# Performance work log

Hardware: AMD Instinct MI355X
Metric: run time of the kernel (lower is better)

The kernel has to match this reference:

```python
import jax, jax.numpy as jnp
import numpy as np

GRID = 7
NB = 2            # boxes per cell
NC = 20           # classes
IS = NB * 4       # start of confidence channels
D = NB * 5 + NC   # 30 channels per cell
B = 8192
L_BOX = 5.0       # threshold_box
L_NEG = 0.5       # threshold_conf_neg


def _bce(logits, target):
    # stable binary_cross_entropy_with_logits, elementwise (reduction handled by caller)
    return jnp.maximum(logits, 0.0) - logits * target + jnp.log1p(jnp.exp(-jnp.abs(logits)))


def _ltrb(xywh):
    xy, wh = xywh[..., :2], xywh[..., 2:4]
    return jnp.concatenate([xy - wh * 0.5, xy + wh * 0.5], axis=-1)


def _iou(a, b):
    lt = jnp.maximum(a[..., :2], b[..., :2])
    rb = jnp.minimum(a[..., 2:], b[..., 2:])
    wh = jnp.maximum(rb - lt, 0.0)
    inter = wh[..., 0] * wh[..., 1]
    area_a = (a[..., 2] - a[..., 0]) * (a[..., 3] - a[..., 1])
    area_b = (b[..., 2] - b[..., 0]) * (b[..., 3] - b[..., 1])
    return inter / (area_a + area_b - inter + 1e-7)


def _box_loss(pb, gb):
    # (x,y) MSE + (sqrt|w|, sqrt h) MSE, summed over the 4 coords -> shape = pb.shape[:-1]
    lxy = jnp.sum((pb[..., :2] - gb[..., :2]) ** 2, axis=-1)
    lwh = jnp.sum((jnp.sqrt(jnp.abs(pb[..., 2:4])) - jnp.sqrt(gb[..., 2:4])) ** 2, axis=-1)
    return lxy + lwh


def _forward(p, g):
    batch = p.shape[0]
    conf_g = g[..., IS]                    # [B,S,S] first gt confidence
    mask_pos = conf_g > 0
    mask_neg = conf_g == 0

    # positive-cell class loss (BCE with logits, sum)
    cls_cell = _bce(p[..., NB * 5:], g[..., NB * 5:]).sum(-1)
    loss_cls_pos = jnp.sum(jnp.where(mask_pos, cls_cell, 0.0))

    # negative-cell confidence loss vs zeros
    neg_cell = _bce(p[..., IS:IS + 2], 0.0).sum(-1)
    loss_conf_neg = jnp.sum(jnp.where(mask_neg, neg_cell, 0.0))

    # per-cell boxes: [B,S,S,NB,4]
    pbox = p[..., :IS].reshape(batch, GRID, GRID, NB, 4)
    gbox = g[..., :IS].reshape(batch, GRID, GRID, NB, 4)
    poff = jnp.concatenate([jax.nn.sigmoid(pbox[..., :2]), pbox[..., 2:]], axis=-1)

    # grid offsets: colrow_index = [col=ds2, row=ds1]; xy = (offxy + colrow) / grid
    row = jnp.broadcast_to(jnp.arange(GRID, dtype=p.dtype)[:, None], (GRID, GRID))
    col = jnp.broadcast_to(jnp.arange(GRID, dtype=p.dtype)[None, :], (GRID, GRID))
    cr = jnp.stack([col, row], axis=-1)[None, :, :, None, :]   # [1,S,S,1,2]

    # IoU matching is done under no_grad in the original -> stop_gradient
    poff_ng = jax.lax.stop_gradient(poff)
    p_ltrb = _ltrb(jnp.concatenate([(poff_ng[..., :2] + cr) / GRID, poff_ng[..., 2:]], -1))
    g_ltrb = _ltrb(jnp.concatenate([(gbox[..., :2] + cr) / GRID, gbox[..., 2:]], -1))
    ious = _iou(p_ltrb[..., :, None, :], g_ltrb[..., None, :, :])   # [B,S,S,NB,NB]
    ind = jnp.argmax(ious, axis=-2)                                  # best pbox per gbox, [B,S,S,NB]

    same_g = jnp.all(gbox[..., 0, :] == gbox[..., 1, :], axis=-1)
    same_ind = ind[..., 0] == ind[..., 1]

    gathered = jnp.take_along_axis(poff, ind[..., :, None], axis=-2)  # poff[ind]
    lossA = _box_loss(gathered[..., 0, :], gbox[..., 0, :])           # identical gt boxes
    lossB = _box_loss(poff, gbox).sum(-1)
    lossC = _box_loss(gathered, gbox).sum(-1)                          # distinct matches
    box_cell = jnp.where(same_g, lossA, jnp.where(same_ind, lossB, lossC))

    pconf = p[..., IS:IS + 2]
    confA = _bce(jnp.take_along_axis(pconf, ind[..., 1:2], axis=-1)[..., 0], 1.0)
    confBC = _bce(pconf, 1.0).sum(-1)
    conf_cell = jnp.where(same_g, confA, confBC)

    loss_box_pos = jnp.sum(jnp.where(mask_pos, box_cell, 0.0))
    loss_conf_pos = jnp.sum(jnp.where(mask_pos, conf_cell, 0.0))

    nb = jnp.asarray(batch, p.dtype)
    loss_box = L_BOX * loss_box_pos / nb
    loss_conf = (loss_conf_pos + L_NEG * loss_conf_neg) / nb
    loss_cls = loss_cls_pos / nb
    return loss_box + loss_conf + loss_cls


def setup_inputs() -> dict:
    key = jax.random.key(0)
    k1, k2, k3, k4 = jax.random.split(key, 4)
    p = jax.random.normal(k1, (B, GRID, GRID, D), dtype=jnp.float32)
    # both conf channels equal (mask semantics), class targets in [0,1]
    boxes = 0.05 + 0.9 * jax.random.uniform(k2, (B, GRID, GRID, IS), dtype=jnp.float32)
    conf = (jax.random.uniform(k3, (B, GRID, GRID, 1)) < 0.3).astype(jnp.float32)
    cls = jax.random.uniform(k4, (B, GRID, GRID, NC), dtype=jnp.float32)
    g = jnp.concatenate([boxes, conf, conf, cls], axis=-1)
    return {"p_yolo_ts": p, "g_yolo_ts": g}


def reference(p_yolo_ts, g_yolo_ts):
    return _forward(p_yolo_ts, g_yolo_ts)
```

## Files before the change

### kernel.cpp

```cpp
#include <hip/hip_runtime.h>
#include <math.h>

#define GRID_N 7
#define DCH 30
#define BATCH 8192
#define NCELL (BATCH * GRID_N * GRID_N)
#define INV_GRID (1.0f / 7.0f)
#define INV_BATCH (1.0f / 8192.0f)
#define TPB 256

__device__ __forceinline__ float bce(float l, float t) {
    return fmaxf(l, 0.0f) - l * t + __logf(1.0f + __expf(-fabsf(l)));
}

__global__ __launch_bounds__(TPB) void yolo_loss_kernel(
        const float* __restrict__ p, const float* __restrict__ g,
        float* __restrict__ out) {
    const int t = threadIdx.x;
    const int cell = blockIdx.x * TPB + t;

    float pv[DCH], gv[DCH];
    {
        const float2* p2 = reinterpret_cast<const float2*>(p) + (long)cell * (DCH / 2);
        const float2* g2 = reinterpret_cast<const float2*>(g) + (long)cell * (DCH / 2);
        float2 tp[DCH / 2], tg[DCH / 2];
        #pragma unroll
        for (int k = 0; k < DCH / 2; ++k) tp[k] = p2[k];
        #pragma unroll
        for (int k = 0; k < DCH / 2; ++k) tg[k] = g2[k];
        #pragma unroll
        for (int k = 0; k < DCH / 2; ++k) { pv[2*k] = tp[k].x; pv[2*k+1] = tp[k].y; }
        #pragma unroll
        for (int k = 0; k < DCH / 2; ++k) { gv[2*k] = tg[k].x; gv[2*k+1] = tg[k].y; }
    }

    const int ij = cell % (GRID_N * GRID_N);
    const float fi = (float)(ij / GRID_N);
    const float fj = (float)(ij % GRID_N);

    const float conf_g = gv[8];
    const float pc0 = pv[8], pc1 = pv[9];

    const float neg_val = 0.5f * (bce(pc0, 0.0f) + bce(pc1, 0.0f));

    const float po0x = 1.0f / (1.0f + __expf(-pv[0]));
    const float po0y = 1.0f / (1.0f + __expf(-pv[1]));
    const float po0w = pv[2], po0h = pv[3];
    const float po1x = 1.0f / (1.0f + __expf(-pv[4]));
    const float po1y = 1.0f / (1.0f + __expf(-pv[5]));
    const float po1w = pv[6], po1h = pv[7];

    const float p0cx = (po0x + fj) * INV_GRID, p0cy = (po0y + fi) * INV_GRID;
    const float p0l = p0cx - po0w * 0.5f, p0t = p0cy - po0h * 0.5f;
    const float p0r = p0cx + po0w * 0.5f, p0b = p0cy + po0h * 0.5f;
    const float pa0 = (p0r - p0l) * (p0b - p0t);
    const float p1cx = (po1x + fj) * INV_GRID, p1cy = (po1y + fi) * INV_GRID;
    const float p1l = p1cx - po1w * 0.5f, p1t = p1cy - po1h * 0.5f;
    const float p1r = p1cx + po1w * 0.5f, p1b = p1cy + po1h * 0.5f;
    const float pa1 = (p1r - p1l) * (p1b - p1t);

    const float g0cx = (gv[0] + fj) * INV_GRID, g0cy = (gv[1] + fi) * INV_GRID;
    const float g0l = g0cx - gv[2] * 0.5f, g0t = g0cy - gv[3] * 0.5f;
    const float g0r = g0cx + gv[2] * 0.5f, g0b = g0cy + gv[3] * 0.5f;
    const float ga0 = (g0r - g0l) * (g0b - g0t);
    const float g1cx = (gv[4] + fj) * INV_GRID, g1cy = (gv[5] + fi) * INV_GRID;
    const float g1l = g1cx - gv[6] * 0.5f, g1t = g1cy - gv[7] * 0.5f;
    const float g1r = g1cx + gv[6] * 0.5f, g1b = g1cy + gv[7] * 0.5f;
    const float ga1 = (g1r - g1l) * (g1b - g1t);

    #define IOU(PL,PT,PR,PB,PAR, GL,GT,GR,GB,GAR)                              \
        ({ float ltx = fmaxf(PL, GL), lty = fmaxf(PT, GT);                     \
           float rbx = fminf(PR, GR), rby = fminf(PB, GB);                     \
           float w_ = fmaxf(rbx - ltx, 0.0f), h_ = fmaxf(rby - lty, 0.0f);     \
           float inter = w_ * h_;                                              \
           inter / (PAR + GAR - inter + 1e-7f); })

    const float iou00 = IOU(p0l,p0t,p0r,p0b,pa0, g0l,g0t,g0r,g0b,ga0);
    const float iou10 = IOU(p1l,p1t,p1r,p1b,pa1, g0l,g0t,g0r,g0b,ga0);
    const float iou01 = IOU(p0l,p0t,p0r,p0b,pa0, g1l,g1t,g1r,g1b,ga1);
    const float iou11 = IOU(p1l,p1t,p1r,p1b,pa1, g1l,g1t,g1r,g1b,ga1);
    #undef IOU

    const bool ind0 = (iou10 > iou00);
    const bool ind1 = (iou11 > iou01);

    const float sg0w = sqrtf(gv[2]), sg0h = sqrtf(gv[3]);
    const float sg1w = sqrtf(gv[6]), sg1h = sqrtf(gv[7]);
    const float sp0w = sqrtf(fabsf(po0w)), sp0h = sqrtf(fabsf(po0h));
    const float sp1w = sqrtf(fabsf(po1w)), sp1h = sqrtf(fabsf(po1h));

    #define BL(PX,PY,SW,SH, GX,GY,SGW,SGH)                                     \
        ({ float dx = PX - GX, dy = PY - GY, dw = SW - SGW, dh = SH - SGH;     \
           dx*dx + dy*dy + dw*dw + dh*dh; })
    const float bl00 = BL(po0x,po0y,sp0w,sp0h, gv[0],gv[1],sg0w,sg0h);
    const float bl10 = BL(po1x,po1y,sp1w,sp1h, gv[0],gv[1],sg0w,sg0h);
    const float bl01 = BL(po0x,po0y,sp0w,sp0h, gv[4],gv[5],sg1w,sg1h);
    const float bl11 = BL(po1x,po1y,sp1w,sp1h, gv[4],gv[5],sg1w,sg1h);
    #undef BL

    const bool same_g = (gv[0] == gv[4]) && (gv[1] == gv[5]) &&
                        (gv[2] == gv[6]) && (gv[3] == gv[7]);
    const bool same_ind = (ind0 == ind1);

    const float sel0 = ind0 ? bl10 : bl00;
    const float sel1 = ind1 ? bl11 : bl01;
    const float lossA = sel0;
    const float lossB = bl00 + bl11;
    const float lossC = sel0 + sel1;
    const float box_cell = same_g ? lossA : (same_ind ? lossB : lossC);

    const float confA = bce(ind1 ? pc1 : pc0, 1.0f);
    const float confBC = bce(pc0, 1.0f) + bce(pc1, 1.0f);
    const float conf_cell = same_g ? confA : confBC;

    float cls = 0.0f;
    #pragma unroll
    for (int c = 10; c < DCH; ++c) cls += bce(pv[c], gv[c]);

    const float pos_val = 5.0f * box_cell + conf_cell + cls;

    float acc = (conf_g == 0.0f) ? neg_val
              : ((conf_g > 0.0f) ? pos_val : 0.0f);

    #pragma unroll
    for (int off = 32; off > 0; off >>= 1) acc += __shfl_down(acc, off, 64);

    __shared__ float red[TPB / 64];
    const int lane = t & 63;
    const int wid = t >> 6;
    if (lane == 0) red[wid] = acc;
    __syncthreads();
    if (t == 0) {
        float s = 0.0f;
        #pragma unroll
        for (int w = 0; w < TPB / 64; ++w) s += red[w];
        atomicAdd(out, s * INV_BATCH);
    }
}

extern "C" void kernel_launch(void* const* d_in, const int* in_sizes, int n_in,
                              void* d_out, int out_size, void* d_ws, size_t ws_size,
                              hipStream_t stream) {
    const float* p = (const float*)d_in[0];
    const float* g = (const float*)d_in[1];
    float* out = (float*)d_out;

    const int grid = NCELL / TPB;
    yolo_loss_kernel<<<grid, TPB, 0, stream>>>(p, g, out);
}
```

Measured before the change: 127.5 us.

## Stage per-block inputs through padded LDS with coalesced float4 loads

```diff
diff --git a/kernel.cpp b/kernel.cpp
--- a/kernel.cpp
+++ b/kernel.cpp
@@ -8,32 +8,71 @@
 #define INV_GRID (1.0f / 7.0f)
 #define INV_BATCH (1.0f / 8192.0f)
 #define TPB 256
+#define NPAIRB (TPB / 2)
+#define F4PB (TPB * DCH / 4)
+#define PSLOT 17
 
 __device__ __forceinline__ float bce(float l, float t) {
     return fmaxf(l, 0.0f) - l * t + __logf(1.0f + __expf(-fabsf(l)));
 }
 
-__global__ __launch_bounds__(TPB) void yolo_loss_kernel(
+__global__ __launch_bounds__(TPB, 4) void yolo_loss_kernel(
         const float* __restrict__ p, const float* __restrict__ g,
         float* __restrict__ out) {
+    __shared__ float4 sbuf4[NPAIRB * PSLOT];
+    float* sbuf = reinterpret_cast<float*>(sbuf4);
+    __shared__ float red[TPB / 64];
+
     const int t = threadIdx.x;
-    const int cell = blockIdx.x * TPB + t;
+    const int blk = blockIdx.x;
+    const int q = t >> 1;
+    const int h = t & 1;
+    const int rbase = q * (PSLOT * 4) + 30 * h;
 
-    float pv[DCH], gv[DCH];
     {
-        const float2* p2 = reinterpret_cast<const float2*>(p) + (long)cell * (DCH / 2);
-        const float2* g2 = reinterpret_cast<const float2*>(g) + (long)cell * (DCH / 2);
-        float2 tp[DCH / 2], tg[DCH / 2];
+        const float4* g4 = reinterpret_cast<const float4*>(g) + (long)blk * F4PB;
         #pragma unroll
-        for (int k = 0; k < DCH / 2; ++k) tp[k] = p2[k];
+        for (int i = 0; i < 8; ++i) {
+            int f = i * TPB + t;
+            if (f < F4PB) {
+                int qq = f / 15;
+                int ss = f - qq * 15;
+                sbuf4[qq * PSLOT + ss] = g4[f];
+            }
+        }
+    }
+    __syncthreads();
+
+    float gv[DCH];
+    #pragma unroll
+    for (int j = 0; j < 15; ++j) {
+        float2 v = *reinterpret_cast<const float2*>(&sbuf[rbase + 2 * j]);
+        gv[2*j] = v.x; gv[2*j+1] = v.y;
+    }
+    __syncthreads();
+
+    {
+        const float4* p4 = reinterpret_cast<const float4*>(p) + (long)blk * F4PB;
         #pragma unroll
-        for (int k = 0; k < DCH / 2; ++k) tg[k] = g2[k];
-        #pragma unroll
-        for (int k = 0; k < DCH / 2; ++k) { pv[2*k] = tp[k].x; pv[2*k+1] = tp[k].y; }
-        #pragma unroll
-        for (int k = 0; k < DCH / 2; ++k) { gv[2*k] = tg[k].x; gv[2*k+1] = tg[k].y; }
+        for (int i = 0; i < 8; ++i) {
+            int f = i * TPB + t;
+            if (f < F4PB) {
+                int qq = f / 15;
+                int ss = f - qq * 15;
+                sbuf4[qq * PSLOT + ss] = p4[f];
+            }
+        }
+    }
+    __syncthreads();
+
+    float pv[DCH];
+    #pragma unroll
+    for (int j = 0; j < 15; ++j) {
+        float2 v = *reinterpret_cast<const float2*>(&sbuf[rbase + 2 * j]);
+        pv[2*j] = v.x; pv[2*j+1] = v.y;
     }
 
+    const int cell = blk * TPB + t;
     const int ij = cell % (GRID_N * GRID_N);
     const float fi = (float)(ij / GRID_N);
     const float fj = (float)(ij % GRID_N);
@@ -125,7 +164,6 @@
     #pragma unroll
     for (int off = 32; off > 0; off >>= 1) acc += __shfl_down(acc, off, 64);
 
-    __shared__ float red[TPB / 64];
     const int lane = t & 63;
     const int wid = t >> 6;
     if (lane == 0) red[wid] = acc;
```

Result: faster. 123.7 us (-2.9%).
